# Performance work log

Measured on AMD Instinct MI355X. Metric: run time of the kernel, lower is better.

Reference implementation:

```python
import jax, jax.numpy as jnp
import numpy as np

N = 50000      # nodes
E = 800000     # edges
G = 512        # graphs in batch
F0 = 92        # orig atom feature len
F = 64         # atom_fea_len
NB = 41        # nbr_fea_len
H = 128        # h_fea_len
NCONV = 3
EPS = 1e-5


def setup_inputs() -> dict:
    key = jax.random.key(0)
    ks = jax.random.split(key, 16)
    s = 0.05
    inp = {
        "x": jax.random.normal(ks[0], (N, F0), jnp.float32),
        "edge_index": jax.random.randint(ks[1], (2, E), 0, N),
        "edge_attr": jax.random.normal(ks[2], (E, NB), jnp.float32),
        "batch": jnp.sort(jax.random.randint(ks[3], (N,), 0, G)),
        # embedding (only applied at the first conv, when x width == F0)
        "emb_W": jax.random.normal(ks[4], (F0, F), jnp.float32) * s,
        "emb_b": jnp.zeros((F,), jnp.float32),
        # per-conv-layer params, stacked on leading axis
        "bn1_g": jnp.ones((NCONV, F), jnp.float32),
        "bn1_b": jnp.zeros((NCONV, F), jnp.float32),
        "bn2_g": jnp.ones((NCONV, F), jnp.float32),
        "bn2_b": jnp.zeros((NCONV, F), jnp.float32),
        "lnf_W": jax.random.normal(ks[5], (NCONV, 2 * F + NB, F), jnp.float32) * s,
        "lnf_b": jnp.zeros((NCONV, F), jnp.float32),
        "lns_W": jax.random.normal(ks[6], (NCONV, 2 * F + NB, F), jnp.float32) * s,
        "lns_b": jnp.zeros((NCONV, F), jnp.float32),
        # readout MLP
        "fc1_W": jax.random.normal(ks[7], (F, H), jnp.float32) * s,
        "fc1_b": jnp.zeros((H,), jnp.float32),
        "out_W": jax.random.normal(ks[8], (H, 1), jnp.float32) * s,
        "out_b": jnp.zeros((1,), jnp.float32),
    }
    return inp


def _batchnorm(x, g, b):
    # training-mode BatchNorm1d: batch stats over node dim, biased variance
    mean = jnp.mean(x, axis=0)
    var = jnp.var(x, axis=0)
    return (x - mean) * jax.lax.rsqrt(var + EPS) * g + b


def _cgconv(x, edge_index, edge_attr, bn1_g, bn1_b, bn2_g, bn2_b, Wf, bf, Ws, bs):
    x = _batchnorm(x, bn1_g, bn1_b)
    # flow='target_to_source': x_i = x[edge_index[0]], x_j = x[edge_index[1]],
    # aggregation scatter-adds messages to edge_index[0]
    src, dst = edge_index[0], edge_index[1]
    z = jnp.concatenate([x[src], x[dst], edge_attr], axis=-1)   # [E, 2F+NB]
    m = jax.nn.sigmoid(z @ Wf + bf) * jax.nn.softplus(z @ Ws + bs)
    agg = jax.ops.segment_sum(m, src, num_segments=x.shape[0])  # [N, F]
    out = _batchnorm(agg, bn2_g, bn2_b) + x
    return jax.nn.softplus(out)


def reference(x, edge_index, edge_attr, batch, emb_W, emb_b,
              bn1_g, bn1_b, bn2_g, bn2_b, lnf_W, lnf_b, lns_W, lns_b,
              fc1_W, fc1_b, out_W, out_b):
    h = x @ emb_W + emb_b  # first conv applies embedding (x width == F0)
    for i in range(NCONV):
        h = _cgconv(h, edge_index, edge_attr,
                    bn1_g[i], bn1_b[i], bn2_g[i], bn2_b[i],
                    lnf_W[i], lnf_b[i], lns_W[i], lns_b[i])
    # global mean pool per graph
    sums = jax.ops.segment_sum(h, batch, num_segments=G)
    cnts = jax.ops.segment_sum(jnp.ones((h.shape[0], 1), h.dtype), batch, num_segments=G)
    crys = sums / jnp.maximum(cnts, 1.0)                         # [G, F]
    crys = jax.nn.softplus(jax.nn.softplus(crys) @ fc1_W + fc1_b)
    return crys @ out_W + out_b                                  # [G, 1]
```

## Files before the change

kernel.cpp:

```cpp
#include <hip/hip_runtime.h>

#define NN 50000
#define NE 800000
#define NG 512
#define F0 92
#define FF 64
#define NB 41
#define HH 128
#define NBLK_SCAN 196

typedef float f4 __attribute__((ext_vector_type(4)));
typedef float f4u __attribute__((ext_vector_type(4), aligned(4)));

__device__ __forceinline__ float softplusf(float x) {
    return fmaxf(x, 0.f) + __logf(1.f + __expf(-fabsf(x)));
}
__device__ __forceinline__ float sigmoidf(float x) {
    return __fdividef(1.f, 1.f + __expf(-x));
}


__global__ __launch_bounds__(256) void hist_kernel(const int* __restrict__ ei,
                                                   int* __restrict__ cnt)
{
    for (int e = blockIdx.x * 256 + threadIdx.x; e < NE; e += gridDim.x * 256)
        atomicAdd(&cnt[ei[e]], 1);
}

__global__ __launch_bounds__(256) void scan1_kernel(const int* __restrict__ cnt,
                                                    int* __restrict__ bsum)
{
    __shared__ int sd[256];
    const int t = threadIdx.x;
    const int idx = blockIdx.x * 256 + t;
    sd[t] = (idx < NN) ? cnt[idx] : 0;
    __syncthreads();
    for (int s = 128; s > 0; s >>= 1) {
        if (t < s) sd[t] += sd[t + s];
        __syncthreads();
    }
    if (t == 0) bsum[blockIdx.x] = sd[0];
}

__global__ __launch_bounds__(256) void scan2_kernel(int* __restrict__ bsum,
                                                    int* __restrict__ rowptr)
{
    __shared__ int sd[256];
    const int t = threadIdx.x;
    const int v = (t < NBLK_SCAN) ? bsum[t] : 0;
    sd[t] = v;
    __syncthreads();
    for (int off = 1; off < 256; off <<= 1) {
        int a = (t >= off) ? sd[t - off] : 0;
        __syncthreads();
        sd[t] += a;
        __syncthreads();
    }
    if (t < NBLK_SCAN) bsum[t] = sd[t] - v;
    if (t == 255) rowptr[NN] = sd[255];
}

__global__ __launch_bounds__(256) void scan3_kernel(const int* __restrict__ cnt,
                                                    const int* __restrict__ bsum,
                                                    int* __restrict__ rowptr,
                                                    int* __restrict__ cursor)
{
    __shared__ int sd[256];
    const int t = threadIdx.x;
    const int idx = blockIdx.x * 256 + t;
    const int v = (idx < NN) ? cnt[idx] : 0;
    sd[t] = v;
    __syncthreads();
    for (int off = 1; off < 256; off <<= 1) {
        int a = (t >= off) ? sd[t - off] : 0;
        __syncthreads();
        sd[t] += a;
        __syncthreads();
    }
    if (idx < NN) {
        const int ex = bsum[blockIdx.x] + sd[t] - v;
        rowptr[idx] = ex;
        cursor[idx] = ex;
    }
}

__global__ __launch_bounds__(256) void scatter_kernel(const int* __restrict__ ei,
                                                      int* __restrict__ cursor,
                                                      int2* __restrict__ sorted)
{
    for (int e = blockIdx.x * 256 + threadIdx.x; e < NE; e += gridDim.x * 256) {
        const int s = ei[e];
        const int pos = atomicAdd(&cursor[s], 1);
        sorted[pos] = make_int2(e, ei[NE + e]);
    }
}


__global__ __launch_bounds__(256) void emb_kernel(
    const float* __restrict__ x, const float* __restrict__ W,
    const float* __restrict__ bias, float* __restrict__ h)
{
    __shared__ float sx[4][F0];
    const int lane = threadIdx.x & 63;
    const int w = threadIdx.x >> 6;
    float wr[F0];
#pragma unroll
    for (int k = 0; k < F0; ++k) wr[k] = W[k * FF + lane];
    const float bv = bias[lane];
    const int nit = NN / 4;
    for (int it = blockIdx.x; it < nit; it += gridDim.x) {
        const int n = it * 4 + w;
        if (lane < 46) {
            sx[w][lane * 2]     = x[n * F0 + lane * 2];
            sx[w][lane * 2 + 1] = x[n * F0 + lane * 2 + 1];
        }
        __syncthreads();
        float acc = bv;
#pragma unroll
        for (int k4 = 0; k4 < F0 / 4; ++k4) {
            float4 q = *(const float4*)&sx[w][k4 * 4];
            acc = fmaf(q.x, wr[k4 * 4 + 0], acc);
            acc = fmaf(q.y, wr[k4 * 4 + 1], acc);
            acc = fmaf(q.z, wr[k4 * 4 + 2], acc);
            acc = fmaf(q.w, wr[k4 * 4 + 3], acc);
        }
        h[n * FF + lane] = acc;
        __syncthreads();
    }
}

__global__ __launch_bounds__(256) void stats_kernel(
    const float* __restrict__ src, float* __restrict__ stats)
{
    __shared__ float sd[2][4][FF];
    const int f = threadIdx.x & 63;
    const int r = threadIdx.x >> 6;
    float s = 0.f, s2 = 0.f;
    for (int n = blockIdx.x * 4 + r; n < NN; n += gridDim.x * 4) {
        float v = src[n * FF + f];
        s += v;
        s2 = fmaf(v, v, s2);
    }
    sd[0][r][f] = s;
    sd[1][r][f] = s2;
    __syncthreads();
    if (threadIdx.x < FF) {
        float ts = sd[0][0][f] + sd[0][1][f] + sd[0][2][f] + sd[0][3][f];
        float t2 = sd[1][0][f] + sd[1][1][f] + sd[1][2][f] + sd[1][3][f];
        atomicAdd(&stats[f], ts);
        atomicAdd(&stats[FF + f], t2);
    }
}

__global__ void finalize_kernel(const float* __restrict__ g, const float* __restrict__ b,
                                float* __restrict__ stats)
{
    const int f = threadIdx.x;
    const float inv = 1.f / (float)NN;
    float mean = stats[f] * inv;
    float var = stats[FF + f] * inv - mean * mean;
    float rstd = rsqrtf(var + 1e-5f);
    float A = rstd * g[f];
    stats[2 * FF + f] = A;
    stats[3 * FF + f] = fmaf(-mean, A, b[f]);
}

__global__ __launch_bounds__(256) void prep_kernel(
    const float* __restrict__ lnfW, const float* __restrict__ lnsW,
    float* __restrict__ wTe)
{
    const int total = 3 * 2 * 64 * 44;
    for (int idx = blockIdx.x * 256 + threadIdx.x; idx < total; idx += gridDim.x * 256) {
        const int k = idx % 44;
        const int lane = (idx / 44) & 63;
        const int m = (idx / (44 * 64)) & 1;
        const int i = idx / (44 * 64 * 2);
        const float* W = (m == 0 ? lnfW : lnsW) + (size_t)i * 169 * FF;
        wTe[idx] = (k < NB) ? W[(2 * FF + k) * FF + lane] : 0.f;
    }
}

__global__ __launch_bounds__(256) void node_kernel(
    const float* __restrict__ h, const float* __restrict__ stats,
    const float* __restrict__ Wf, const float* __restrict__ Ws,
    const float* __restrict__ bf, const float* __restrict__ bs,
    float* __restrict__ xn, float* __restrict__ pS, float* __restrict__ pD)
{
    __shared__ float sx[4][FF];
    const int lane = threadIdx.x & 63;
    const int w = threadIdx.x >> 6;
    const float* W = (w < 2) ? Wf : Ws;
    const int rowbase = (w & 1) * FF;
    float wr[FF];
#pragma unroll
    for (int k = 0; k < FF; ++k) wr[k] = W[(rowbase + k) * FF + lane];
    const float A = stats[2 * FF + lane];
    const float B = stats[3 * FF + lane];
    float bias = 0.f;
    if (w == 0) bias = bf[lane];
    if (w == 2) bias = bs[lane];
    float* outp = ((w & 1) ? pD : pS) + ((w >> 1) & 1);
    for (int n = blockIdx.x; n < NN; n += gridDim.x) {
        const float xv = fmaf(h[n * FF + lane], A, B);
        if (w == 0) xn[n * FF + lane] = xv;
        sx[w][lane] = xv;
        __syncthreads();
        float acc = bias;
#pragma unroll
        for (int k4 = 0; k4 < FF / 4; ++k4) {
            float4 q = *(const float4*)&sx[w][k4 * 4];
            acc = fmaf(q.x, wr[k4 * 4 + 0], acc);
            acc = fmaf(q.y, wr[k4 * 4 + 1], acc);
            acc = fmaf(q.z, wr[k4 * 4 + 2], acc);
            acc = fmaf(q.w, wr[k4 * 4 + 3], acc);
        }
        outp[(size_t)n * 128 + 2 * lane] = acc;
        __syncthreads();
    }
}

__global__ __launch_bounds__(256) __attribute__((amdgpu_waves_per_eu(4, 4)))
void edge_kernel(
    const int2* __restrict__ sorted, const float* __restrict__ ea,
    const int* __restrict__ rowptr, const float* __restrict__ wTe,
    const float* __restrict__ pS, const float* __restrict__ pD,
    float* __restrict__ agg)
{
    const int lane = threadIdx.x & 63;
    const float* wtf = wTe + (size_t)lane * 44;
    const float* wts = wTe + (size_t)(FF + lane) * 44;
    f4 wfr[11], wsr[11];
#pragma unroll
    for (int k4 = 0; k4 < 11; ++k4) {
        wfr[k4] = *(const f4*)&wtf[k4 * 4];
        wsr[k4] = *(const f4*)&wts[k4 * 4];
        asm volatile("" : "+v"(wfr[k4]), "+v"(wsr[k4]));
    }
    const int nwave = (gridDim.x * blockDim.x) >> 6;
    const int wid = (blockIdx.x * blockDim.x + threadIdx.x) >> 6;
    for (int n0 = wid; n0 < NN; n0 += nwave) {
        const int n = __builtin_amdgcn_readfirstlane(n0);
        const int rs = rowptr[n];
        const int re = rowptr[n + 1];
        const float2 gS = *(const float2*)(pS + (size_t)n * 128 + 2 * lane);
        float acc = 0.f;
        for (int e = rs; e < re; ++e) {
            const int2 sd2 = sorted[e];
            const int se = sd2.x;
            const int dst = sd2.y;
            const float2 gD = *(const float2*)(pD + (size_t)dst * 128 + 2 * lane);
            const float* er = ea + (size_t)se * NB;
            float aF0 = gS.x, aF1 = gD.x, aS0 = gS.y, aS1 = gD.y;
#pragma unroll
            for (int k4 = 0; k4 < 10; k4 += 2) {
                const f4u q0 = *(const f4u*)(er + k4 * 4);
                const f4u q1 = *(const f4u*)(er + k4 * 4 + 4);
                aF0 = fmaf(q0.x, wfr[k4].x, aF0);     aS0 = fmaf(q0.x, wsr[k4].x, aS0);
                aF0 = fmaf(q0.y, wfr[k4].y, aF0);     aS0 = fmaf(q0.y, wsr[k4].y, aS0);
                aF0 = fmaf(q0.z, wfr[k4].z, aF0);     aS0 = fmaf(q0.z, wsr[k4].z, aS0);
                aF0 = fmaf(q0.w, wfr[k4].w, aF0);     aS0 = fmaf(q0.w, wsr[k4].w, aS0);
                aF1 = fmaf(q1.x, wfr[k4 + 1].x, aF1); aS1 = fmaf(q1.x, wsr[k4 + 1].x, aS1);
                aF1 = fmaf(q1.y, wfr[k4 + 1].y, aF1); aS1 = fmaf(q1.y, wsr[k4 + 1].y, aS1);
                aF1 = fmaf(q1.z, wfr[k4 + 1].z, aF1); aS1 = fmaf(q1.z, wsr[k4 + 1].z, aS1);
                aF1 = fmaf(q1.w, wfr[k4 + 1].w, aF1); aS1 = fmaf(q1.w, wsr[k4 + 1].w, aS1);
            }
            const float q40 = er[40];
            aF0 = fmaf(q40, wfr[10].x, aF0);
            aS0 = fmaf(q40, wsr[10].x, aS0);
            acc += sigmoidf(aF0 + aF1) * softplusf(aS0 + aS1);
        }
        agg[(size_t)n * FF + lane] = acc;
    }
}

__global__ __launch_bounds__(256) void update_kernel(
    const float* __restrict__ agg, const float* __restrict__ xn,
    const float* __restrict__ stats, float* __restrict__ h,
    const int* __restrict__ batch, float* __restrict__ pool,
    float* __restrict__ pcnt, const int do_pool)
{
    const int total = NN * FF;
    for (int idx = blockIdx.x * blockDim.x + threadIdx.x; idx < total;
         idx += gridDim.x * blockDim.x) {
        const int f = idx & 63;
        const int n = idx >> 6;
        const float A = stats[2 * FF + f];
        const float B = stats[3 * FF + f];
        const float v = softplusf(fmaf(agg[idx], A, B) + xn[idx]);
        if (do_pool) {
            const int g = batch[n];
            unsafeAtomicAdd(&pool[g * FF + f], v);
            if (f == 0) unsafeAtomicAdd(&pcnt[g], 1.f);
        } else {
            h[idx] = v;
        }
    }
}

__global__ __launch_bounds__(128) void readout_kernel(
    const float* __restrict__ pool, const float* __restrict__ pcnt,
    const float* __restrict__ fc1W, const float* __restrict__ fc1b,
    const float* __restrict__ outW, const float* __restrict__ outb,
    float* __restrict__ out)
{
    __shared__ float sp[FF];
    __shared__ float red[2];
    const int g = blockIdx.x;
    const int t = threadIdx.x;
    if (t < FF) {
        const float c = fmaxf(pcnt[g], 1.f);
        sp[t] = softplusf(pool[g * FF + t] / c);
    }
    __syncthreads();
    float a = fc1b[t];
#pragma unroll
    for (int k = 0; k < FF; ++k) a = fmaf(sp[k], fc1W[k * HH + t], a);
    float o = softplusf(a) * outW[t];
#pragma unroll
    for (int off = 32; off > 0; off >>= 1) o += __shfl_down(o, off, 64);
    if ((t & 63) == 0) red[t >> 6] = o;
    __syncthreads();
    if (t == 0) out[g] = red[0] + red[1] + outb[0];
}

extern "C" void kernel_launch(void* const* d_in, const int* in_sizes, int n_in,
                              void* d_out, int out_size, void* d_ws, size_t ws_size,
                              hipStream_t stream)
{
    const float* x     = (const float*)d_in[0];
    const int*   ei    = (const int*)  d_in[1];
    const float* ea    = (const float*)d_in[2];
    const int*   batch = (const int*)  d_in[3];
    const float* embW  = (const float*)d_in[4];
    const float* embb  = (const float*)d_in[5];
    const float* bn1g  = (const float*)d_in[6];
    const float* bn1b  = (const float*)d_in[7];
    const float* bn2g  = (const float*)d_in[8];
    const float* bn2b  = (const float*)d_in[9];
    const float* lnfW  = (const float*)d_in[10];
    const float* lnfb  = (const float*)d_in[11];
    const float* lnsW  = (const float*)d_in[12];
    const float* lnsb  = (const float*)d_in[13];
    const float* fc1W  = (const float*)d_in[14];
    const float* fc1b  = (const float*)d_in[15];
    const float* outW  = (const float*)d_in[16];
    const float* outb  = (const float*)d_in[17];

    float* ws    = (float*)d_ws;
    float* h     = ws;
    float* xn    = h    + (size_t)NN * FF;
    float* pS    = xn   + (size_t)NN * FF;
    float* pD    = pS   + (size_t)NN * 128;
    float* agg   = pD   + (size_t)NN * 128;
    float* stats = agg  + (size_t)NN * FF;
    float* pool  = stats + 4 * FF;
    float* pcnt  = pool + (size_t)NG * FF;
    float* wTe   = pcnt + NG;
    int*   cnt    = (int*)(wTe + 3 * 2 * 64 * 44);
    int*   rowptr = cnt + NN;
    int*   cursor = rowptr + NN + 2;
    int*   bsum   = cursor + NN;
    int2*  sorted = (int2*)(bsum + 256);

    hipMemsetAsync(cnt, 0, NN * sizeof(int), stream);
    hist_kernel<<<2048, 256, 0, stream>>>(ei, cnt);
    scan1_kernel<<<NBLK_SCAN, 256, 0, stream>>>(cnt, bsum);
    scan2_kernel<<<1, 256, 0, stream>>>(bsum, rowptr);
    scan3_kernel<<<NBLK_SCAN, 256, 0, stream>>>(cnt, bsum, rowptr, cursor);
    scatter_kernel<<<2048, 256, 0, stream>>>(ei, cursor, sorted);

    hipMemsetAsync(pool, 0, (NG * FF + NG) * sizeof(float), stream);
    prep_kernel<<<66, 256, 0, stream>>>(lnfW, lnsW, wTe);
    emb_kernel<<<1024, 256, 0, stream>>>(x, embW, embb, h);

    for (int i = 0; i < 3; ++i) {
        const float* Wf  = lnfW + (size_t)i * 169 * FF;
        const float* Wsp = lnsW + (size_t)i * 169 * FF;
        hipMemsetAsync(stats, 0, 2 * FF * sizeof(float), stream);
        stats_kernel<<<256, 256, 0, stream>>>(h, stats);
        finalize_kernel<<<1, 64, 0, stream>>>(bn1g + i * FF, bn1b + i * FF, stats);
        node_kernel<<<1024, 256, 0, stream>>>(h, stats, Wf, Wsp,
                                              lnfb + i * FF, lnsb + i * FF, xn, pS, pD);
        edge_kernel<<<1024, 256, 0, stream>>>(sorted, ea, rowptr,
                                              wTe + (size_t)i * 2 * FF * 44, pS, pD, agg);
        hipMemsetAsync(stats, 0, 2 * FF * sizeof(float), stream);
        stats_kernel<<<256, 256, 0, stream>>>(agg, stats);
        finalize_kernel<<<1, 64, 0, stream>>>(bn2g + i * FF, bn2b + i * FF, stats);
        update_kernel<<<2048, 256, 0, stream>>>(agg, xn, stats, h, batch, pool, pcnt,
                                                (i == 2) ? 1 : 0);
    }
    readout_kernel<<<NG, HH, 0, stream>>>(pool, pcnt, fc1W, fc1b, outW, outb, (float*)d_out);
}
```

Before: 1.083 ms.

## Switch edge kernel to edge-per-lane mapping with transposed sorted edge features

Edge features are permuted into source-sorted order and transposed to a feature-major layout once up front. The edge kernel then assigns one edge per lane, keeps the edge-feature weights in LDS, and computes 16-feature tiles in registers. Messages are staged in LDS, combined within the wave across edges that share a source, and written to agg with atomics, which now needs a memset first. This replaces the per-node loop, where each lane re-read the same unaligned 41-float edge row, with coalesced loads, at the cost of a transpose kernel, float atomics and higher register pressure.

```diff
diff --git a/kernel.cpp b/kernel.cpp
--- a/kernel.cpp
+++ b/kernel.cpp
@@ -8,6 +8,7 @@
 #define NB 41
 #define HH 128
 #define NBLK_SCAN 196
+#define NBATCH (NE / 64)
 
 typedef float f4 __attribute__((ext_vector_type(4)));
 typedef float f4u __attribute__((ext_vector_type(4), aligned(4)));
@@ -86,13 +87,28 @@
 
 __global__ __launch_bounds__(256) void scatter_kernel(const int* __restrict__ ei,
                                                       int* __restrict__ cursor,
-                                                      int2* __restrict__ sorted)
+                                                      int* __restrict__ perm,
+                                                      int* __restrict__ srcS,
+                                                      int* __restrict__ dstS)
 {
     for (int e = blockIdx.x * 256 + threadIdx.x; e < NE; e += gridDim.x * 256) {
         const int s = ei[e];
         const int pos = atomicAdd(&cursor[s], 1);
-        sorted[pos] = make_int2(e, ei[NE + e]);
-    }
+        perm[pos] = e;
+        srcS[pos] = s;
+        dstS[pos] = ei[NE + e];
+    }
+}
+
+__global__ __launch_bounds__(256) void tr_kernel(const float* __restrict__ ea,
+                                                 const int* __restrict__ perm,
+                                                 float* __restrict__ eaT)
+{
+    const int pos = blockIdx.x * 256 + threadIdx.x;
+    if (pos >= NE) return;
+    const float* row = ea + (size_t)perm[pos] * NB;
+#pragma unroll
+    for (int k = 0; k < NB; ++k) eaT[(size_t)k * NE + pos] = row[k];
 }
 
 
@@ -167,16 +183,15 @@
 
 __global__ __launch_bounds__(256) void prep_kernel(
     const float* __restrict__ lnfW, const float* __restrict__ lnsW,
-    float* __restrict__ wTe)
-{
-    const int total = 3 * 2 * 64 * 44;
+    float* __restrict__ wT)
+{
+    const int total = 3 * NB * 128;
     for (int idx = blockIdx.x * 256 + threadIdx.x; idx < total; idx += gridDim.x * 256) {
-        const int k = idx % 44;
-        const int lane = (idx / 44) & 63;
-        const int m = (idx / (44 * 64)) & 1;
-        const int i = idx / (44 * 64 * 2);
-        const float* W = (m == 0 ? lnfW : lnsW) + (size_t)i * 169 * FF;
-        wTe[idx] = (k < NB) ? W[(2 * FF + k) * FF + lane] : 0.f;
+        const int f = idx & 127;
+        const int k = (idx >> 7) % NB;
+        const int i = idx / (128 * NB);
+        const float* W = (f < FF ? lnfW : lnsW) + (size_t)i * 169 * FF;
+        wT[idx] = W[(2 * FF + k) * FF + (f & 63)];
     }
 }
 
@@ -221,55 +236,82 @@
 
 __global__ __launch_bounds__(256) __attribute__((amdgpu_waves_per_eu(4, 4)))
 void edge_kernel(
-    const int2* __restrict__ sorted, const float* __restrict__ ea,
-    const int* __restrict__ rowptr, const float* __restrict__ wTe,
+    const float* __restrict__ eaT, const int* __restrict__ srcS,
+    const int* __restrict__ dstS, const float* __restrict__ wT,
     const float* __restrict__ pS, const float* __restrict__ pD,
     float* __restrict__ agg)
 {
-    const int lane = threadIdx.x & 63;
-    const float* wtf = wTe + (size_t)lane * 44;
-    const float* wts = wTe + (size_t)(FF + lane) * 44;
-    f4 wfr[11], wsr[11];
-#pragma unroll
-    for (int k4 = 0; k4 < 11; ++k4) {
-        wfr[k4] = *(const f4*)&wtf[k4 * 4];
-        wsr[k4] = *(const f4*)&wts[k4 * 4];
-        asm volatile("" : "+v"(wfr[k4]), "+v"(wsr[k4]));
-    }
-    const int nwave = (gridDim.x * blockDim.x) >> 6;
-    const int wid = (blockIdx.x * blockDim.x + threadIdx.x) >> 6;
-    for (int n0 = wid; n0 < NN; n0 += nwave) {
-        const int n = __builtin_amdgcn_readfirstlane(n0);
-        const int rs = rowptr[n];
-        const int re = rowptr[n + 1];
-        const float2 gS = *(const float2*)(pS + (size_t)n * 128 + 2 * lane);
-        float acc = 0.f;
-        for (int e = rs; e < re; ++e) {
-            const int2 sd2 = sorted[e];
-            const int se = sd2.x;
-            const int dst = sd2.y;
-            const float2 gD = *(const float2*)(pD + (size_t)dst * 128 + 2 * lane);
-            const float* er = ea + (size_t)se * NB;
-            float aF0 = gS.x, aF1 = gD.x, aS0 = gS.y, aS1 = gD.y;
-#pragma unroll
-            for (int k4 = 0; k4 < 10; k4 += 2) {
-                const f4u q0 = *(const f4u*)(er + k4 * 4);
-                const f4u q1 = *(const f4u*)(er + k4 * 4 + 4);
-                aF0 = fmaf(q0.x, wfr[k4].x, aF0);     aS0 = fmaf(q0.x, wsr[k4].x, aS0);
-                aF0 = fmaf(q0.y, wfr[k4].y, aF0);     aS0 = fmaf(q0.y, wsr[k4].y, aS0);
-                aF0 = fmaf(q0.z, wfr[k4].z, aF0);     aS0 = fmaf(q0.z, wsr[k4].z, aS0);
-                aF0 = fmaf(q0.w, wfr[k4].w, aF0);     aS0 = fmaf(q0.w, wsr[k4].w, aS0);
-                aF1 = fmaf(q1.x, wfr[k4 + 1].x, aF1); aS1 = fmaf(q1.x, wsr[k4 + 1].x, aS1);
-                aF1 = fmaf(q1.y, wfr[k4 + 1].y, aF1); aS1 = fmaf(q1.y, wsr[k4 + 1].y, aS1);
-                aF1 = fmaf(q1.z, wfr[k4 + 1].z, aF1); aS1 = fmaf(q1.z, wsr[k4 + 1].z, aS1);
-                aF1 = fmaf(q1.w, wfr[k4 + 1].w, aF1); aS1 = fmaf(q1.w, wsr[k4 + 1].w, aS1);
+    __shared__ float wlds[NB * 128];
+    __shared__ float mld[4][64 * 17 + 4];
+    __shared__ int   sld[4][64];
+    const int t = threadIdx.x;
+    const int lane = t & 63;
+    const int w = t >> 6;
+    for (int i = t; i < NB * 128; i += 256) wlds[i] = wT[i];
+    __syncthreads();
+
+    const int nw = (gridDim.x * blockDim.x) >> 6;
+    const int gw = (blockIdx.x * blockDim.x + t) >> 6;
+    const int le = lane >> 4, lf = lane & 15;
+
+    for (int b = gw; b < NBATCH; b += nw) {
+        const int pos = b * 64 + lane;
+        const int srcv = srcS[pos];
+        const int dstv = dstS[pos];
+        sld[w][lane] = srcv;
+        float e[NB];
+#pragma unroll
+        for (int k = 0; k < NB; ++k) e[k] = eaT[(size_t)k * NE + pos];
+
+        for (int tile = 0; tile < 4; ++tile) {
+            const int f0 = tile * 16;
+            float accF[16], accS[16];
+#pragma unroll
+            for (int j = 0; j < 16; ++j) { accF[j] = 0.f; accS[j] = 0.f; }
+#pragma unroll
+            for (int k = 0; k < NB; ++k) {
+                const f4* wg = (const f4*)&wlds[k * 128 + f0];
+                const f4* wc = (const f4*)&wlds[k * 128 + FF + f0];
+#pragma unroll
+                for (int q = 0; q < 4; ++q) {
+                    const f4 g = wg[q], c = wc[q];
+                    accF[4 * q + 0] = fmaf(e[k], g.x, accF[4 * q + 0]);
+                    accF[4 * q + 1] = fmaf(e[k], g.y, accF[4 * q + 1]);
+                    accF[4 * q + 2] = fmaf(e[k], g.z, accF[4 * q + 2]);
+                    accF[4 * q + 3] = fmaf(e[k], g.w, accF[4 * q + 3]);
+                    accS[4 * q + 0] = fmaf(e[k], c.x, accS[4 * q + 0]);
+                    accS[4 * q + 1] = fmaf(e[k], c.y, accS[4 * q + 1]);
+                    accS[4 * q + 2] = fmaf(e[k], c.z, accS[4 * q + 2]);
+                    accS[4 * q + 3] = fmaf(e[k], c.w, accS[4 * q + 3]);
+                }
             }
-            const float q40 = er[40];
-            aF0 = fmaf(q40, wfr[10].x, aF0);
-            aS0 = fmaf(q40, wsr[10].x, aS0);
-            acc += sigmoidf(aF0 + aF1) * softplusf(aS0 + aS1);
+            const float* pSr = pS + (size_t)srcv * 128 + f0 * 2;
+            const float* pDr = pD + (size_t)dstv * 128 + f0 * 2;
+#pragma unroll
+            for (int q = 0; q < 8; ++q) {
+                const f4u sv = *(const f4u*)(pSr + 4 * q);
+                const f4u dv = *(const f4u*)(pDr + 4 * q);
+                const float mF0 = accF[2 * q]     + sv.x + dv.x;
+                const float mS0 = accS[2 * q]     + sv.y + dv.y;
+                const float mF1 = accF[2 * q + 1] + sv.z + dv.z;
+                const float mS1 = accS[2 * q + 1] + sv.w + dv.w;
+                mld[w][lane * 17 + 2 * q]     = sigmoidf(mF0) * softplusf(mS0);
+                mld[w][lane * 17 + 2 * q + 1] = sigmoidf(mF1) * softplusf(mS1);
+            }
+            for (int s = 0; s < 16; ++s) {
+                const int eidx = s * 4 + le;
+                float v = mld[w][eidx * 17 + lf];
+                const int sA = sld[w][eidx];
+                const int sB = (le <= 2) ? sld[w][eidx + 1] : -1;
+                const int sC = (le <= 1) ? sld[w][eidx + 2] : -1;
+                const float t1 = __shfl_down(v, 16);
+                if (sB == sA) v += t1;
+                const float t2 = __shfl_down(v, 32);
+                if (sC == sA) v += t2;
+                const bool head = (le == 0) || (sld[w][eidx - 1] != sA);
+                if (head) unsafeAtomicAdd(&agg[(size_t)sA * FF + f0 + lf], v);
+            }
         }
-        agg[(size_t)n * FF + lane] = acc;
     }
 }
 
@@ -355,22 +397,26 @@
     float* stats = agg  + (size_t)NN * FF;
     float* pool  = stats + 4 * FF;
     float* pcnt  = pool + (size_t)NG * FF;
-    float* wTe   = pcnt + NG;
-    int*   cnt    = (int*)(wTe + 3 * 2 * 64 * 44);
+    float* wT    = pcnt + NG;
+    int*   cnt    = (int*)(wT + 3 * NB * 128);
     int*   rowptr = cnt + NN;
     int*   cursor = rowptr + NN + 2;
     int*   bsum   = cursor + NN;
-    int2*  sorted = (int2*)(bsum + 256);
+    int*   perm   = bsum + 256;
+    int*   srcS   = perm + NE;
+    int*   dstS   = srcS + NE;
+    float* eaT    = (float*)(dstS + NE);
 
     hipMemsetAsync(cnt, 0, NN * sizeof(int), stream);
     hist_kernel<<<2048, 256, 0, stream>>>(ei, cnt);
     scan1_kernel<<<NBLK_SCAN, 256, 0, stream>>>(cnt, bsum);
     scan2_kernel<<<1, 256, 0, stream>>>(bsum, rowptr);
     scan3_kernel<<<NBLK_SCAN, 256, 0, stream>>>(cnt, bsum, rowptr, cursor);
-    scatter_kernel<<<2048, 256, 0, stream>>>(ei, cursor, sorted);
+    scatter_kernel<<<2048, 256, 0, stream>>>(ei, cursor, perm, srcS, dstS);
+    tr_kernel<<<(NE + 255) / 256, 256, 0, stream>>>(ea, perm, eaT);
 
     hipMemsetAsync(pool, 0, (NG * FF + NG) * sizeof(float), stream);
-    prep_kernel<<<66, 256, 0, stream>>>(lnfW, lnsW, wTe);
+    prep_kernel<<<62, 256, 0, stream>>>(lnfW, lnsW, wT);
     emb_kernel<<<1024, 256, 0, stream>>>(x, embW, embb, h);
 
     for (int i = 0; i < 3; ++i) {
@@ -381,8 +427,9 @@
         finalize_kernel<<<1, 64, 0, stream>>>(bn1g + i * FF, bn1b + i * FF, stats);
         node_kernel<<<1024, 256, 0, stream>>>(h, stats, Wf, Wsp,
                                               lnfb + i * FF, lnsb + i * FF, xn, pS, pD);
-        edge_kernel<<<1024, 256, 0, stream>>>(sorted, ea, rowptr,
-                                              wTe + (size_t)i * 2 * FF * 44, pS, pD, agg);
+        hipMemsetAsync(agg, 0, (size_t)NN * FF * sizeof(float), stream);
+        edge_kernel<<<NBATCH / 4, 256, 0, stream>>>(eaT, srcS, dstS,
+                                                    wT + (size_t)i * NB * 128, pS, pD, agg);
         hipMemsetAsync(stats, 0, 2 * FF * sizeof(float), stream);
         stats_kernel<<<256, 256, 0, stream>>>(agg, stats);
         finalize_kernel<<<1, 64, 0, stream>>>(bn2g + i * FF, bn2b + i * FF, stats);
```

New measurement: 1.205 ms. 11.2% more time.
